# Kernel optimization log

Hardware: AMD Instinct MI355X
Metric: run time of the kernel (lower is better)

Reference implementation:

```python
import jax, jax.numpy as jnp
import numpy as np

B, S, D, H, FF = 1, 4096, 512, 8, 2048
DK = D // H
EPS = 1e-6


def layer_norm(x, alpha, beta):
    # Original LayerNorm: scalar alpha/beta, torch.std (ddof=1), eps added to std.
    mean = jnp.mean(x, axis=-1, keepdims=True)
    var = jnp.var(x, axis=-1, keepdims=True) * (D / (D - 1))  # Bessel-corrected, like torch.std
    std = jnp.sqrt(var)
    return alpha * (x - mean) / (std + EPS) + beta


def setup_inputs() -> dict:
    key = jax.random.key(0)
    ks = jax.random.split(key, 12)
    sd = 1.0 / np.sqrt(D)
    sf = 1.0 / np.sqrt(FF)
    inp = {
        "x": jax.random.normal(ks[0], (B, S, D), jnp.float32),
        "mask": jnp.ones((1, 1, 1, S), jnp.int32),
        "wq": jax.random.uniform(ks[1], (D, D), jnp.float32, -sd, sd),
        "bq": jnp.zeros((D,), jnp.float32),
        "wk": jax.random.uniform(ks[2], (D, D), jnp.float32, -sd, sd),
        "bk": jnp.zeros((D,), jnp.float32),
        "wv": jax.random.uniform(ks[3], (D, D), jnp.float32, -sd, sd),
        "bv": jnp.zeros((D,), jnp.float32),
        "wo": jax.random.uniform(ks[4], (D, D), jnp.float32, -sd, sd),
        "bo": jnp.zeros((D,), jnp.float32),
        "w1": jax.random.uniform(ks[5], (D, FF), jnp.float32, -sd, sd),
        "b1": jnp.zeros((FF,), jnp.float32),
        "w2": jax.random.uniform(ks[6], (FF, D), jnp.float32, -sf, sf),
        "b2": jnp.zeros((D,), jnp.float32),
        "ln1_a": jnp.ones((1,), jnp.float32),
        "ln1_b": jnp.zeros((1,), jnp.float32),
        "ln2_a": jnp.ones((1,), jnp.float32),
        "ln2_b": jnp.zeros((1,), jnp.float32),
    }
    return inp


def reference(x, mask, wq, bq, wk, bk, wv, bv, wo, bo, w1, b1, w2, b2,
              ln1_a, ln1_b, ln2_a, ln2_b):
    # --- pre-LN self-attention sublayer with residual ---
    h = layer_norm(x, ln1_a, ln1_b)
    q = (h @ wq + bq).reshape(B, S, H, DK).transpose(0, 2, 1, 3)  # [B,H,S,dk]
    k = (h @ wk + bk).reshape(B, S, H, DK).transpose(0, 2, 1, 3)
    v = (h @ wv + bv).reshape(B, S, H, DK).transpose(0, 2, 1, 3)
    scores = jnp.einsum('bhqd,bhkd->bhqk', q, k) / np.sqrt(DK)     # [B,H,S,S]
    scores = jnp.where(mask == 0, jnp.float32(-1e9), scores)
    probs = jax.nn.softmax(scores, axis=-1)
    attn = jnp.einsum('bhqk,bhkd->bhqd', probs, v)                 # [B,H,S,dk]
    attn = attn.transpose(0, 2, 1, 3).reshape(B, S, D)
    x = x + (attn @ wo + bo)
    # --- pre-LN feed-forward sublayer with residual ---
    h2 = layer_norm(x, ln2_a, ln2_b)
    ff = jax.nn.relu(h2 @ w1 + b1) @ w2 + b2
    return x + ff
```

## Files before the change

### kernel.cpp

```cpp
#include <hip/hip_runtime.h>
#include <hip/hip_bf16.h>

#define S_LEN 4096
#define D_DIM 512
#define H_NUM 8
#define DK_DIM 64
#define FF_DIM 2048
#define QLD 1536

typedef __attribute__((ext_vector_type(8))) short short8;
typedef __attribute__((ext_vector_type(4))) float f32x4;
typedef __attribute__((ext_vector_type(4))) ushort us4;

#if __has_builtin(__builtin_amdgcn_exp2f)
#define EXP2F __builtin_amdgcn_exp2f
#else
#define EXP2F exp2f
#endif

__device__ __forceinline__ ushort f2bf(float f) {
    union { float f; uint u; } v; v.f = f;
    uint r = v.u + 0x7FFF + ((v.u >> 16) & 1);
    return (ushort)(r >> 16);
}

__device__ __forceinline__ void gload_lds16(const void* g, void* l) {
    __builtin_amdgcn_global_load_lds(
        (const __attribute__((address_space(1))) void*)g,
        (__attribute__((address_space(3))) void*)l,
        16, 0, 0);
}

#define MFMA16(a, b, c) __builtin_amdgcn_mfma_f32_16x16x32_bf16(a, b, c, 0, 0, 0)

__global__ __launch_bounds__(256) void prep_all(
    const float* __restrict__ wq, const float* __restrict__ wk,
    const float* __restrict__ wv, const float* __restrict__ wo,
    const float* __restrict__ w1, const float* __restrict__ w2,
    const float* __restrict__ bq, const float* __restrict__ bk,
    const float* __restrict__ bv, const int* __restrict__ mask,
    ushort* __restrict__ wqkvt, ushort* __restrict__ wot,
    ushort* __restrict__ w1t, ushort* __restrict__ w2t,
    float* __restrict__ bqkv, float* __restrict__ mbias)
{
    __shared__ float t[32][33];
    const int bid = blockIdx.x, tid = threadIdx.x;
    if (bid < 3072) {
        const float* src; ushort* dst; int K, N, tx, ty;
        if (bid < 1024) {
            int wsel = bid >> 8, id = bid & 255;
            src = wsel == 0 ? wq : wsel == 1 ? wk : wsel == 2 ? wv : wo;
            dst = wsel == 0 ? wqkvt : wsel == 1 ? wqkvt + 512 * 512
                : wsel == 2 ? wqkvt + 1024 * 512 : wot;
            K = 512; N = 512; tx = id & 15; ty = id >> 4;
        } else if (bid < 2048) {
            int id = bid - 1024; src = w1; dst = w1t;
            K = 512; N = 2048; tx = id & 63; ty = id >> 6;
        } else {
            int id = bid - 2048; src = w2; dst = w2t;
            K = 2048; N = 512; tx = id & 15; ty = id >> 4;
        }
        int gn = tx * 32, gk = ty * 32;
        int lx = tid & 31, ly = tid >> 5;
#pragma unroll
        for (int i = 0; i < 32; i += 8)
            t[ly + i][lx] = src[(size_t)(gk + ly + i) * N + gn + lx];
        __syncthreads();
#pragma unroll
        for (int i = 0; i < 32; i += 8)
            dst[(size_t)(gn + ly + i) * K + gk + lx] = f2bf(t[lx][ly + i]);
    } else {
        int i = (bid - 3072) * 256 + tid;
        if (i < 512)       bqkv[i] = bq[i];
        else if (i < 1024) bqkv[i] = bk[i - 512];
        else if (i < 1536) bqkv[i] = bv[i - 1024];
        mbias[i] = mask[i] ? 0.0f : -1e9f;
    }
}

__global__ __launch_bounds__(256) void ln1_kernel(
    const float* __restrict__ x,
    const float* __restrict__ aP, const float* __restrict__ bP,
    ushort* __restrict__ out)
{
    const int row = blockIdx.x;
    const int d = threadIdx.x * 2;
    float2 v = *(const float2*)(x + (size_t)row * D_DIM + d);
    float sum = v.x + v.y;
    float sq  = v.x * v.x + v.y * v.y;
#pragma unroll
    for (int off = 1; off < 64; off <<= 1) {
        sum += __shfl_xor(sum, off);
        sq  += __shfl_xor(sq, off);
    }
    __shared__ float ssum[4], ssq[4];
    int wid = threadIdx.x >> 6;
    if ((threadIdx.x & 63) == 0) { ssum[wid] = sum; ssq[wid] = sq; }
    __syncthreads();
    sum = ssum[0] + ssum[1] + ssum[2] + ssum[3];
    sq  = ssq[0] + ssq[1] + ssq[2] + ssq[3];
    float mean = sum * (1.0f / D_DIM);
    float var  = (sq - (float)D_DIM * mean * mean) * (1.0f / (D_DIM - 1));
    var = fmaxf(var, 0.0f);
    float scale = aP[0] / (sqrtf(var) + 1e-6f);
    float beta  = bP[0];
    ushort2 o;
    o.x = f2bf((v.x - mean) * scale + beta);
    o.y = f2bf((v.y - mean) * scale + beta);
    *(ushort2*)(out + (size_t)row * D_DIM + d) = o;
}

__global__ __launch_bounds__(256) void ln2_fused(
    const float* __restrict__ x, const float* __restrict__ bo,
    const float* __restrict__ p0, const float* __restrict__ p1,
    const float* __restrict__ aP, const float* __restrict__ bP,
    float* __restrict__ x2, ushort* __restrict__ h2)
{
    const int row = blockIdx.x;
    const int d = threadIdx.x * 2;
    const size_t idx = (size_t)row * D_DIM + d;
    float2 xv = *(const float2*)(x + idx);
    float2 a0 = *(const float2*)(p0 + idx);
    float2 a1 = *(const float2*)(p1 + idx);
    float2 bb = *(const float2*)(bo + d);
    float2 v;
    v.x = xv.x + a0.x + a1.x + bb.x;
    v.y = xv.y + a0.y + a1.y + bb.y;
    *(float2*)(x2 + idx) = v;
    float sum = v.x + v.y;
    float sq  = v.x * v.x + v.y * v.y;
#pragma unroll
    for (int off = 1; off < 64; off <<= 1) {
        sum += __shfl_xor(sum, off);
        sq  += __shfl_xor(sq, off);
    }
    __shared__ float ssum[4], ssq[4];
    int wid = threadIdx.x >> 6;
    if ((threadIdx.x & 63) == 0) { ssum[wid] = sum; ssq[wid] = sq; }
    __syncthreads();
    sum = ssum[0] + ssum[1] + ssum[2] + ssum[3];
    sq  = ssq[0] + ssq[1] + ssq[2] + ssq[3];
    float mean = sum * (1.0f / D_DIM);
    float var  = (sq - (float)D_DIM * mean * mean) * (1.0f / (D_DIM - 1));
    var = fmaxf(var, 0.0f);
    float scale = aP[0] / (sqrtf(var) + 1e-6f);
    float beta  = bP[0];
    ushort2 o;
    o.x = f2bf((v.x - mean) * scale + beta);
    o.y = f2bf((v.y - mean) * scale + beta);
    *(ushort2*)(h2 + idx) = o;
}

__global__ __launch_bounds__(256, 2) void gemm_mfma128(
    const ushort* __restrict__ A, const ushort* __restrict__ Bt,
    const float* __restrict__ bias,
    ushort* __restrict__ outB, ushort* __restrict__ outVT,
    int M, int N, int K, int relu)
{
    __shared__ ushort As[2][2][128][32];
    __shared__ ushort Bs[2][2][128][32];
    const int tid = threadIdx.x;
    const int w = tid >> 6, lane = tid & 63;
    const int l15 = lane & 15, quad = lane >> 4;
    const int wm = w >> 1, wn = w & 1;
    const int sw = (l15 >> 1) & 3;
    const int swc = ((lane & 3) ^ ((lane >> 3) & 3)) * 16;
    const int m0 = blockIdx.y * 128, n0 = blockIdx.x * 128;

    f32x4 acc[4][4] = {};

    const char* gA  = (const char*)(A  + (size_t)(m0 + 32 * w + (lane >> 2)) * K) + swc;
    const char* gA2 = gA + (size_t)16 * K * 2;
    const char* gB  = (const char*)(Bt + (size_t)(n0 + 32 * w + (lane >> 2)) * K) + swc;
    const char* gB2 = gB + (size_t)16 * K * 2;

    auto stage = [&](int b) {
        gload_lds16(gA,       &As[b][0][32 * w][0]);
        gload_lds16(gA + 64,  &As[b][1][32 * w][0]);
        gload_lds16(gA2,      &As[b][0][32 * w + 16][0]);
        gload_lds16(gA2 + 64, &As[b][1][32 * w + 16][0]);
        gload_lds16(gB,       &Bs[b][0][32 * w][0]);
        gload_lds16(gB + 64,  &Bs[b][1][32 * w][0]);
        gload_lds16(gB2,      &Bs[b][0][32 * w + 16][0]);
        gload_lds16(gB2 + 64, &Bs[b][1][32 * w + 16][0]);
        gA += 128; gA2 += 128; gB += 128; gB2 += 128;
    };

    stage(0);
    const int nit = K >> 6;
    for (int t = 0; t < nit; ++t) {
        __syncthreads();
        if (t + 1 < nit) stage((t + 1) & 1);
        const int b = t & 1;
#pragma unroll
        for (int ks = 0; ks < 2; ++ks) {
            short8 af[4], bf[4];
#pragma unroll
            for (int i = 0; i < 4; ++i) {
                af[i] = *(const short8*)&As[b][ks][64 * wm + i * 16 + l15][(quad ^ sw) * 8];
                bf[i] = *(const short8*)&Bs[b][ks][64 * wn + i * 16 + l15][(quad ^ sw) * 8];
            }
#pragma unroll
            for (int mt = 0; mt < 4; ++mt)
#pragma unroll
                for (int nt = 0; nt < 4; ++nt)
                    acc[mt][nt] = MFMA16(af[mt], bf[nt], acc[mt][nt]);
        }
    }

    if (outVT && n0 >= 1024) {
#pragma unroll
        for (int mt = 0; mt < 4; ++mt)
#pragma unroll
            for (int nt = 0; nt < 4; ++nt) {
                int nn = n0 + 64 * wn + nt * 16 + l15;
                int mmb = m0 + 64 * wm + mt * 16 + quad * 4;
                us4 pk;
#pragma unroll
                for (int r = 0; r < 4; ++r)
                    pk[r] = (short)f2bf(acc[mt][nt][r] + bias[nn]);
                *(us4*)(outVT + (size_t)(nn - 1024) * S_LEN + mmb) = pk;
            }
        return;
    }

    ushort (*Es)[32][68] = (ushort (*)[32][68])&As[0][0][0][0];
    __syncthreads();
#pragma unroll
    for (int h = 0; h < 2; ++h) {
#pragma unroll
        for (int mt = 2 * h; mt < 2 * h + 2; ++mt)
#pragma unroll
            for (int nt = 0; nt < 4; ++nt)
#pragma unroll
                for (int r = 0; r < 4; ++r) {
                    float v = acc[mt][nt][r] + bias[n0 + 64 * wn + nt * 16 + l15];
                    if (relu) v = fmaxf(v, 0.0f);
                    Es[w][(mt & 1) * 16 + quad * 4 + r][nt * 16 + l15] = f2bf(v);
                }
#pragma unroll
        for (int p2 = 0; p2 < 4; ++p2) {
            int row = p2 * 8 + (lane >> 3);
            int col = (lane & 7) * 8;
            short8 vv = *(const short8*)&Es[w][row][col];
            *(short8*)(outB + (size_t)(m0 + 64 * wm + h * 32 + row) * N
                             + n0 + 64 * wn + col) = vv;
        }
    }
}

__global__ __launch_bounds__(256) void gemm_mfma(
    const ushort* __restrict__ A, const ushort* __restrict__ Bt,
    float* __restrict__ outF,
    int M, int N, int K, int ksl)
{
    __shared__ ushort As[2][2][128][32];
    __shared__ ushort Bs[2][2][64][32];
    const int tid = threadIdx.x;
    const int w = tid >> 6, lane = tid & 63;
    const int l15 = lane & 15, quad = lane >> 4;
    const int sw = (l15 >> 1) & 3;
    const int swc = ((lane & 3) ^ ((lane >> 3) & 3)) * 16;
    const int m0 = blockIdx.y * 128, n0 = blockIdx.x * 64;
    const int kz = blockIdx.z;
    const int kbeg = kz * ksl;

    f32x4 acc[2][4] = {};

    const char* gA  = (const char*)(A  + (size_t)(m0 + 32 * w + (lane >> 2)) * K + kbeg) + swc;
    const char* gA2 = gA + (size_t)16 * K * 2;
    const char* gB  = (const char*)(Bt + (size_t)(n0 + 16 * w + (lane >> 2)) * K + kbeg) + swc;

    auto stage = [&](int b) {
        gload_lds16(gA,       &As[b][0][32 * w][0]);
        gload_lds16(gA + 64,  &As[b][1][32 * w][0]);
        gload_lds16(gA2,      &As[b][0][32 * w + 16][0]);
        gload_lds16(gA2 + 64, &As[b][1][32 * w + 16][0]);
        gload_lds16(gB,       &Bs[b][0][16 * w][0]);
        gload_lds16(gB + 64,  &Bs[b][1][16 * w][0]);
        gA += 128; gA2 += 128; gB += 128;
    };

    stage(0);
    const int nit = ksl >> 6;
    for (int t = 0; t < nit; ++t) {
        __syncthreads();
        if (t + 1 < nit) stage((t + 1) & 1);
        const int b = t & 1;
#pragma unroll
        for (int ks = 0; ks < 2; ++ks) {
            short8 a0 = *(const short8*)&As[b][ks][32 * w + l15][(quad ^ sw) * 8];
            short8 a1 = *(const short8*)&As[b][ks][32 * w + 16 + l15][(quad ^ sw) * 8];
            short8 b0 = *(const short8*)&Bs[b][ks][0 * 16 + l15][(quad ^ sw) * 8];
            short8 b1 = *(const short8*)&Bs[b][ks][1 * 16 + l15][(quad ^ sw) * 8];
            short8 b2 = *(const short8*)&Bs[b][ks][2 * 16 + l15][(quad ^ sw) * 8];
            short8 b3 = *(const short8*)&Bs[b][ks][3 * 16 + l15][(quad ^ sw) * 8];
            acc[0][0] = MFMA16(a0, b0, acc[0][0]);
            acc[0][1] = MFMA16(a0, b1, acc[0][1]);
            acc[0][2] = MFMA16(a0, b2, acc[0][2]);
            acc[0][3] = MFMA16(a0, b3, acc[0][3]);
            acc[1][0] = MFMA16(a1, b0, acc[1][0]);
            acc[1][1] = MFMA16(a1, b1, acc[1][1]);
            acc[1][2] = MFMA16(a1, b2, acc[1][2]);
            acc[1][3] = MFMA16(a1, b3, acc[1][3]);
        }
    }

    float* of = outF + (size_t)kz * M * N;
#pragma unroll
    for (int mt = 0; mt < 2; ++mt)
#pragma unroll
        for (int nt = 0; nt < 4; ++nt)
#pragma unroll
            for (int r = 0; r < 4; ++r) {
                int mm = m0 + 32 * w + mt * 16 + quad * 4 + r;
                int nn = n0 + nt * 16 + l15;
                of[(size_t)mm * N + nn] = acc[mt][nt][r];
            }
}

__global__ __launch_bounds__(256, 3) void flash_mfma(
    const ushort* __restrict__ qkv, const ushort* __restrict__ vbt,
    const float* __restrict__ mbias, ushort* __restrict__ at_bf)
{
    __shared__ ushort Ks[2][128][32];
    __shared__ ushort Vt[4][64][32];
    __shared__ ushort Pld[4][64][40];

    const int bid = blockIdx.x;
    const int head = bid & 7;
    const int q0 = (bid >> 3) * 64;
    const int tid = threadIdx.x;
    const int w = tid >> 6, lane = tid & 63;
    const int l15 = lane & 15, quad = lane >> 4;
    const int hoff = head * DK_DIM;
    const int sw = (l15 >> 1) & 3;
    const int swc = ((lane & 3) ^ ((lane >> 3) & 3)) * 16;

    short8 qf[2][4];
#pragma unroll
    for (int ks = 0; ks < 2; ++ks)
#pragma unroll
        for (int nt = 0; nt < 4; ++nt)
            qf[ks][nt] = *(const short8*)(qkv
                + (size_t)(q0 + nt * 16 + l15) * QLD + hoff + ks * 32 + quad * 8);

    const char* gk0 = (const char*)(qkv + (size_t)(32 * w + (lane >> 2)) * QLD + 512 + hoff) + swc;
    const char* gv0 = (const char*)(vbt + (size_t)(lane >> 2) * S_LEN + w * 32) + swc;

    const short8 ones = {0x3F80, 0x3F80, 0x3F80, 0x3F80,
                         0x3F80, 0x3F80, 0x3F80, 0x3F80};
    f32x4 oacc[4][4] = {};
    f32x4 lacc[4] = {};

    for (int t = 0; t < S_LEN / 128; ++t) {
        const int ktg = t * 128;
        __syncthreads();
        {
            const char* gk = gk0 + (size_t)ktg * (QLD * 2);
            gload_lds16(gk,                             &Ks[0][32 * w][0]);
            gload_lds16(gk + (size_t)16 * QLD * 2,      &Ks[0][32 * w + 16][0]);
            gload_lds16(gk + 64,                        &Ks[1][32 * w][0]);
            gload_lds16(gk + (size_t)16 * QLD * 2 + 64, &Ks[1][32 * w + 16][0]);
            const char* gv = gv0 + ktg * 2;
            gload_lds16(gv,                          &Vt[w][0][0]);
            gload_lds16(gv + (size_t)16 * S_LEN * 2, &Vt[w][16][0]);
            gload_lds16(gv + (size_t)32 * S_LEN * 2, &Vt[w][32][0]);
            gload_lds16(gv + (size_t)48 * S_LEN * 2, &Vt[w][48][0]);
        }
        __syncthreads();

#pragma unroll
        for (int kh = 0; kh < 2; ++kh) {
            f32x4 sacc[4] = {};
#pragma unroll
            for (int ks = 0; ks < 2; ++ks) {
                short8 kf = *(const short8*)&Ks[ks][32 * w + kh * 16 + l15][(quad ^ sw) * 8];
#pragma unroll
                for (int nt = 0; nt < 4; ++nt)
                    sacc[nt] = MFMA16(kf, qf[ks][nt], sacc[nt]);
            }
            f32x4 mb = *(const f32x4*)&mbias[ktg + 32 * w + kh * 16 + quad * 4];
#pragma unroll
            for (int nt = 0; nt < 4; ++nt) {
                us4 pk;
#pragma unroll
                for (int r = 0; r < 4; ++r) {
                    float pv = EXP2F(fmaf(sacc[nt][r], 0.18033688011112042f, mb[r]));
                    pk[r] = (ushort)(__float_as_uint(pv) >> 16);
                }
                *(us4*)&Pld[w][nt * 16 + l15][kh * 16 + quad * 4] = pk;
            }
        }

        short8 bvr[4];
#pragma unroll
        for (int nt = 0; nt < 4; ++nt)
            bvr[nt] = *(const short8*)&Vt[w][nt * 16 + l15][(quad ^ sw) * 8];
#pragma unroll
        for (int mt = 0; mt < 4; ++mt) {
            short8 ap = *(const short8*)&Pld[w][mt * 16 + l15][quad * 8];
            lacc[mt] = MFMA16(ap, ones, lacc[mt]);
#pragma unroll
            for (int nt = 0; nt < 4; ++nt)
                oacc[mt][nt] = MFMA16(ap, bvr[nt], oacc[mt][nt]);
        }
    }

    float* Ored = (float*)&Pld[0][0][0];
    float* lred = (float*)&Ks[0][0][0];
    const int qloc = tid >> 4, dk4 = (tid & 15) * 4;
#pragma unroll
    for (int mt = 0; mt < 4; ++mt) {
        __syncthreads();
        if (mt == 0 && l15 == 0) {
#pragma unroll
            for (int m2 = 0; m2 < 4; ++m2)
#pragma unroll
                for (int r = 0; r < 4; ++r)
                    lred[w * 64 + m2 * 16 + quad * 4 + r] = lacc[m2][r];
        }
#pragma unroll
        for (int nt = 0; nt < 4; ++nt)
#pragma unroll
            for (int r = 0; r < 4; ++r)
                Ored[(w * 16 + quad * 4 + r) * 68 + nt * 16 + l15] = oacc[mt][nt][r];
        __syncthreads();
        f32x4 s = *(const f32x4*)&Ored[qloc * 68 + dk4];
#pragma unroll
        for (int ww = 1; ww < 4; ++ww)
            s += *(const f32x4*)&Ored[(ww * 16 + qloc) * 68 + dk4];
        float l = lred[mt * 16 + qloc] + lred[64 + mt * 16 + qloc]
                + lred[128 + mt * 16 + qloc] + lred[192 + mt * 16 + qloc];
        float inv = 1.0f / l;
        us4 pk;
#pragma unroll
        for (int j = 0; j < 4; ++j) pk[j] = (short)f2bf(s[j] * inv);
        *(us4*)&at_bf[(size_t)(q0 + mt * 16 + qloc) * D_DIM + hoff + dk4] = pk;
    }
}

__global__ __launch_bounds__(256) void ff2_combine(
    const float* __restrict__ x2, const float* __restrict__ b2,
    const float* __restrict__ p0, const float* __restrict__ p1,
    float* __restrict__ out)
{
    size_t i = ((size_t)blockIdx.x * 256 + threadIdx.x) * 4;
    f32x4 a  = *(const f32x4*)(x2 + i);
    f32x4 q0 = *(const f32x4*)(p0 + i);
    f32x4 q1 = *(const f32x4*)(p1 + i);
    f32x4 bb = *(const f32x4*)(b2 + (int)(i & 511));
    f32x4 r = a + q0 + q1 + bb;
    *(f32x4*)(out + i) = r;
}

extern "C" void kernel_launch(void* const* d_in, const int* in_sizes, int n_in,
                              void* d_out, int out_size, void* d_ws, size_t ws_size,
                              hipStream_t stream) {
    (void)in_sizes; (void)n_in; (void)out_size; (void)ws_size;
    const float* x    = (const float*)d_in[0];
    const int*   mask = (const int*)d_in[1];
    const float* wq = (const float*)d_in[2];
    const float* bq = (const float*)d_in[3];
    const float* wk = (const float*)d_in[4];
    const float* bk = (const float*)d_in[5];
    const float* wv = (const float*)d_in[6];
    const float* bv = (const float*)d_in[7];
    const float* wo = (const float*)d_in[8];
    const float* bo = (const float*)d_in[9];
    const float* w1 = (const float*)d_in[10];
    const float* b1 = (const float*)d_in[11];
    const float* w2 = (const float*)d_in[12];
    const float* b2 = (const float*)d_in[13];
    const float* ln1a = (const float*)d_in[14];
    const float* ln1b = (const float*)d_in[15];
    const float* ln2a = (const float*)d_in[16];
    const float* ln2b = (const float*)d_in[17];
    float* out = (float*)d_out;

    const size_t SD = (size_t)S_LEN * D_DIM;
    char* p = (char*)d_ws;
    ushort* wqkvt = (ushort*)p; p += (size_t)1536 * 512 * 2;
    ushort* wot   = (ushort*)p; p += (size_t)512 * 512 * 2;
    ushort* w1t   = (ushort*)p; p += (size_t)2048 * 512 * 2;
    ushort* w2t   = (ushort*)p; p += (size_t)512 * 2048 * 2;
    float*  bqkv  = (float*)p;  p += 1536 * 4;
    float*  mbias = (float*)p;  p += 4096 * 4;
    ushort* h_bf  = (ushort*)p; p += SD * 2;
    ushort* qkv   = (ushort*)p; p += (size_t)4096 * 1536 * 2;
    ushort* vbt   = (ushort*)p; p += SD * 2;
    ushort* at_bf = (ushort*)p; p += SD * 2;
    float*  x2    = (float*)p;  p += SD * 4;
    ushort* h2    = (ushort*)p; p += SD * 2;
    ushort* ff1   = (ushort*)p; p += (size_t)4096 * 2048 * 2;
    float* wopart  = (float*)h_bf;
    float* ff2part = (float*)h_bf;

    dim3 blk(256);

    prep_all<<<dim3(3088), blk, 0, stream>>>(wq, wk, wv, wo, w1, w2, bq, bk, bv,
                                             mask, wqkvt, wot, w1t, w2t, bqkv, mbias);

    ln1_kernel<<<dim3(S_LEN), blk, 0, stream>>>(x, ln1a, ln1b, h_bf);

    gemm_mfma128<<<dim3(12, 32), blk, 0, stream>>>(
        h_bf, wqkvt, bqkv, qkv, vbt, S_LEN, 1536, 512, 0);

    flash_mfma<<<dim3(512), blk, 0, stream>>>(qkv, vbt, mbias, at_bf);

    gemm_mfma<<<dim3(8, 32, 2), blk, 0, stream>>>(
        at_bf, wot, wopart, S_LEN, 512, 512, 256);

    ln2_fused<<<dim3(S_LEN), blk, 0, stream>>>(x, bo, wopart, wopart + SD,
                                               ln2a, ln2b, x2, h2);

    gemm_mfma128<<<dim3(16, 32), blk, 0, stream>>>(
        h2, w1t, b1, ff1, nullptr, S_LEN, 2048, 512, 1);

    gemm_mfma<<<dim3(8, 32, 2), blk, 0, stream>>>(
        ff1, w2t, ff2part, S_LEN, 512, 2048, 1024);

    ff2_combine<<<dim3(2048), blk, 0, stream>>>(
        x2, b2, ff2part, ff2part + SD, out);
}
```

Measured before the change: 245.6 us.

## Replace async LDS double-buffering with register-prefetched single-buffer staging in GEMM and flash

In both the 128x128 GEMM and the flash-attention kernel, direct global-to-LDS loads into double buffers are replaced by loads of the next tile into registers, which are written to a single LDS buffer at the top of each iteration. An extra barrier at the end of each iteration protects that buffer. The GEMM's shared memory is unioned with the epilogue staging buffer, and its occupancy hint is dropped. The flash kernel's occupancy hint goes from 3 to 2 blocks, and its epilogue barriers are trimmed. This trades LDS footprint and async loads for more registers and an extra barrier per iteration.

```diff
diff --git a/kernel.cpp b/kernel.cpp
--- a/kernel.cpp
+++ b/kernel.cpp
@@ -151,14 +151,16 @@
     *(ushort2*)(h2 + idx) = o;
 }
 
-__global__ __launch_bounds__(256, 2) void gemm_mfma128(
+__global__ __launch_bounds__(256) void gemm_mfma128(
     const ushort* __restrict__ A, const ushort* __restrict__ Bt,
     const float* __restrict__ bias,
     ushort* __restrict__ outB, ushort* __restrict__ outVT,
     int M, int N, int K, int relu)
 {
-    __shared__ ushort As[2][2][128][32];
-    __shared__ ushort Bs[2][2][128][32];
+    __shared__ union {
+        struct { ushort As[2][128][32]; ushort Bs[2][128][32]; } s;
+        ushort Es[4][32][68];
+    } u;
     const int tid = threadIdx.x;
     const int w = tid >> 6, lane = tid & 63;
     const int l15 = lane & 15, quad = lane >> 4;
@@ -174,31 +176,35 @@
     const char* gB  = (const char*)(Bt + (size_t)(n0 + 32 * w + (lane >> 2)) * K) + swc;
     const char* gB2 = gB + (size_t)16 * K * 2;
 
-    auto stage = [&](int b) {
-        gload_lds16(gA,       &As[b][0][32 * w][0]);
-        gload_lds16(gA + 64,  &As[b][1][32 * w][0]);
-        gload_lds16(gA2,      &As[b][0][32 * w + 16][0]);
-        gload_lds16(gA2 + 64, &As[b][1][32 * w + 16][0]);
-        gload_lds16(gB,       &Bs[b][0][32 * w][0]);
-        gload_lds16(gB + 64,  &Bs[b][1][32 * w][0]);
-        gload_lds16(gB2,      &Bs[b][0][32 * w + 16][0]);
-        gload_lds16(gB2 + 64, &Bs[b][1][32 * w + 16][0]);
+    short8 ra[4], rb[4];
+    auto preload = [&]() {
+        ra[0] = *(const short8*)gA;        ra[1] = *(const short8*)gA2;
+        ra[2] = *(const short8*)(gA + 64); ra[3] = *(const short8*)(gA2 + 64);
+        rb[0] = *(const short8*)gB;        rb[1] = *(const short8*)gB2;
+        rb[2] = *(const short8*)(gB + 64); rb[3] = *(const short8*)(gB2 + 64);
         gA += 128; gA2 += 128; gB += 128; gB2 += 128;
     };
 
-    stage(0);
+    preload();
     const int nit = K >> 6;
     for (int t = 0; t < nit; ++t) {
-        __syncthreads();
-        if (t + 1 < nit) stage((t + 1) & 1);
-        const int b = t & 1;
+        *(short8*)(&u.s.As[0][32 * w][0]      + lane * 8) = ra[0];
+        *(short8*)(&u.s.As[0][32 * w + 16][0] + lane * 8) = ra[1];
+        *(short8*)(&u.s.As[1][32 * w][0]      + lane * 8) = ra[2];
+        *(short8*)(&u.s.As[1][32 * w + 16][0] + lane * 8) = ra[3];
+        *(short8*)(&u.s.Bs[0][32 * w][0]      + lane * 8) = rb[0];
+        *(short8*)(&u.s.Bs[0][32 * w + 16][0] + lane * 8) = rb[1];
+        *(short8*)(&u.s.Bs[1][32 * w][0]      + lane * 8) = rb[2];
+        *(short8*)(&u.s.Bs[1][32 * w + 16][0] + lane * 8) = rb[3];
+        __syncthreads();
+        if (t + 1 < nit) preload();
 #pragma unroll
         for (int ks = 0; ks < 2; ++ks) {
             short8 af[4], bf[4];
 #pragma unroll
             for (int i = 0; i < 4; ++i) {
-                af[i] = *(const short8*)&As[b][ks][64 * wm + i * 16 + l15][(quad ^ sw) * 8];
-                bf[i] = *(const short8*)&Bs[b][ks][64 * wn + i * 16 + l15][(quad ^ sw) * 8];
+                af[i] = *(const short8*)&u.s.As[ks][64 * wm + i * 16 + l15][(quad ^ sw) * 8];
+                bf[i] = *(const short8*)&u.s.Bs[ks][64 * wn + i * 16 + l15][(quad ^ sw) * 8];
             }
 #pragma unroll
             for (int mt = 0; mt < 4; ++mt)
@@ -206,6 +212,7 @@
                 for (int nt = 0; nt < 4; ++nt)
                     acc[mt][nt] = MFMA16(af[mt], bf[nt], acc[mt][nt]);
         }
+        __syncthreads();
     }
 
     if (outVT && n0 >= 1024) {
@@ -224,8 +231,6 @@
         return;
     }
 
-    ushort (*Es)[32][68] = (ushort (*)[32][68])&As[0][0][0][0];
-    __syncthreads();
 #pragma unroll
     for (int h = 0; h < 2; ++h) {
 #pragma unroll
@@ -236,16 +241,18 @@
                 for (int r = 0; r < 4; ++r) {
                     float v = acc[mt][nt][r] + bias[n0 + 64 * wn + nt * 16 + l15];
                     if (relu) v = fmaxf(v, 0.0f);
-                    Es[w][(mt & 1) * 16 + quad * 4 + r][nt * 16 + l15] = f2bf(v);
+                    u.Es[w][(mt & 1) * 16 + quad * 4 + r][nt * 16 + l15] = f2bf(v);
                 }
+        __syncthreads();
 #pragma unroll
         for (int p2 = 0; p2 < 4; ++p2) {
             int row = p2 * 8 + (lane >> 3);
             int col = (lane & 7) * 8;
-            short8 vv = *(const short8*)&Es[w][row][col];
+            short8 vv = *(const short8*)&u.Es[w][row][col];
             *(short8*)(outB + (size_t)(m0 + 64 * wm + h * 32 + row) * N
                              + n0 + 64 * wn + col) = vv;
         }
+        __syncthreads();
     }
 }
 
@@ -319,7 +326,7 @@
             }
 }
 
-__global__ __launch_bounds__(256, 3) void flash_mfma(
+__global__ __launch_bounds__(256, 2) void flash_mfma(
     const ushort* __restrict__ qkv, const ushort* __restrict__ vbt,
     const float* __restrict__ mbias, ushort* __restrict__ at_bf)
 {
@@ -348,27 +355,39 @@
     const char* gk0 = (const char*)(qkv + (size_t)(32 * w + (lane >> 2)) * QLD + 512 + hoff) + swc;
     const char* gv0 = (const char*)(vbt + (size_t)(lane >> 2) * S_LEN + w * 32) + swc;
 
+    short8 rk[4], rv[4];
+    auto preload = [&](int ktg) {
+        const char* gk = gk0 + (size_t)ktg * (QLD * 2);
+        rk[0] = *(const short8*)gk;
+        rk[1] = *(const short8*)(gk + (size_t)16 * QLD * 2);
+        rk[2] = *(const short8*)(gk + 64);
+        rk[3] = *(const short8*)(gk + (size_t)16 * QLD * 2 + 64);
+        const char* gv = gv0 + ktg * 2;
+        rv[0] = *(const short8*)gv;
+        rv[1] = *(const short8*)(gv + (size_t)16 * S_LEN * 2);
+        rv[2] = *(const short8*)(gv + (size_t)32 * S_LEN * 2);
+        rv[3] = *(const short8*)(gv + (size_t)48 * S_LEN * 2);
+    };
+    preload(0);
+
     const short8 ones = {0x3F80, 0x3F80, 0x3F80, 0x3F80,
                          0x3F80, 0x3F80, 0x3F80, 0x3F80};
     f32x4 oacc[4][4] = {};
     f32x4 lacc[4] = {};
 
-    for (int t = 0; t < S_LEN / 128; ++t) {
+    const int NIT = S_LEN / 128;
+    for (int t = 0; t < NIT; ++t) {
+        *(short8*)(&Ks[0][32 * w][0]      + lane * 8) = rk[0];
+        *(short8*)(&Ks[0][32 * w + 16][0] + lane * 8) = rk[1];
+        *(short8*)(&Ks[1][32 * w][0]      + lane * 8) = rk[2];
+        *(short8*)(&Ks[1][32 * w + 16][0] + lane * 8) = rk[3];
+        *(short8*)(&Vt[w][0][0]  + lane * 8) = rv[0];
+        *(short8*)(&Vt[w][16][0] + lane * 8) = rv[1];
+        *(short8*)(&Vt[w][32][0] + lane * 8) = rv[2];
+        *(short8*)(&Vt[w][48][0] + lane * 8) = rv[3];
+        __syncthreads();
+        if (t + 1 < NIT) preload((t + 1) * 128);
         const int ktg = t * 128;
-        __syncthreads();
-        {
-            const char* gk = gk0 + (size_t)ktg * (QLD * 2);
-            gload_lds16(gk,                             &Ks[0][32 * w][0]);
-            gload_lds16(gk + (size_t)16 * QLD * 2,      &Ks[0][32 * w + 16][0]);
-            gload_lds16(gk + 64,                        &Ks[1][32 * w][0]);
-            gload_lds16(gk + (size_t)16 * QLD * 2 + 64, &Ks[1][32 * w + 16][0]);
-            const char* gv = gv0 + ktg * 2;
-            gload_lds16(gv,                          &Vt[w][0][0]);
-            gload_lds16(gv + (size_t)16 * S_LEN * 2, &Vt[w][16][0]);
-            gload_lds16(gv + (size_t)32 * S_LEN * 2, &Vt[w][32][0]);
-            gload_lds16(gv + (size_t)48 * S_LEN * 2, &Vt[w][48][0]);
-        }
-        __syncthreads();
 
 #pragma unroll
         for (int kh = 0; kh < 2; ++kh) {
@@ -405,21 +424,22 @@
             for (int nt = 0; nt < 4; ++nt)
                 oacc[mt][nt] = MFMA16(ap, bvr[nt], oacc[mt][nt]);
         }
+        __syncthreads();
     }
 
     float* Ored = (float*)&Pld[0][0][0];
     float* lred = (float*)&Ks[0][0][0];
     const int qloc = tid >> 4, dk4 = (tid & 15) * 4;
+    if (l15 == 0) {
+#pragma unroll
+        for (int m2 = 0; m2 < 4; ++m2)
+#pragma unroll
+            for (int r = 0; r < 4; ++r)
+                lred[w * 64 + m2 * 16 + quad * 4 + r] = lacc[m2][r];
+    }
 #pragma unroll
     for (int mt = 0; mt < 4; ++mt) {
-        __syncthreads();
-        if (mt == 0 && l15 == 0) {
-#pragma unroll
-            for (int m2 = 0; m2 < 4; ++m2)
-#pragma unroll
-                for (int r = 0; r < 4; ++r)
-                    lred[w * 64 + m2 * 16 + quad * 4 + r] = lacc[m2][r];
-        }
+        if (mt) __syncthreads();
 #pragma unroll
         for (int nt = 0; nt < 4; ++nt)
 #pragma unroll
```

Measured after the change: 239.0 us. -2.7%, faster.
